# Optimization experiments

Hardware: AMD Instinct MI355X
Metric: run time of the kernel (lower is better)

The kernel has to match this reference:

```python
import jax, jax.numpy as jnp
import numpy as np

# ---- static configuration (mirrors resource grid / pilot pattern) ----
NB_SYMB = 14                 # num_ofdm_symbols
NSC = 4096                   # fft_size == num_effective_subcarriers (dc_null=False)
PILOT_SYMBS = np.array([2, 11], dtype=np.int32)  # OFDM symbols carrying pilots
STEP = 2                     # subcarriers_step (comb-2, offset 0)
M = NSC // STEP              # pilots per pilot OFDM symbol (constant, as asserted)
BATCH = 512
SC = np.arange(0, NSC, STEP, dtype=np.int32)     # pilot subcarrier positions
ROWS = np.repeat(PILOT_SYMBS, M)                 # flattened pilot (symbol, sc) map,
COLS = np.tile(SC, len(PILOT_SYMBS))             # frequency-then-time ordering


def _time_interp_tables():
    """Replicates _generate_time_interpolation_index_ with numpy (static)."""
    u = PILOT_SYMBS
    idx = np.empty((2, NB_SYMB), dtype=np.int32)
    nf = np.empty(NB_SYMB, dtype=np.float32)
    if u[0] != 0:
        idx[:, : u[0]] = u[0]
        nf[: u[0]] = 0.0
    idx[:, u[-1]:] = u[-1]
    nf[u[-1]:] = 0.0
    for i in range(len(u) - 1):
        idx[0, u[i]: u[i + 1]] = u[i]
        idx[1, u[i]: u[i + 1]] = u[i + 1]
        d = u[i + 1] - u[i]
        nf[u[i]: u[i + 1]] = np.arange(d, dtype=np.float32) / d
    return idx[0], idx[1], nf

IDX0, IDX1, NORM = _time_interp_tables()


def setup_inputs() -> dict:
    key = jax.random.key(0)
    k1, k2 = jax.random.split(key)
    shape = (BATCH, len(PILOT_SYMBS) * M)
    return {
        "h_pilots_real": jax.random.normal(k1, shape, dtype=jnp.float32),
        "h_pilots_imag": jax.random.normal(k2, shape, dtype=jnp.float32),
    }


def reference(h_pilots_real, h_pilots_imag):
    pilots = (h_pilots_real + 1j * h_pilots_imag).astype(jnp.complex64)  # [B, P]
    B = pilots.shape[0]
    # scatter_nd of pilot estimates into the full grid [T, F, B]
    updates = pilots.T  # [P, B]
    grid = jnp.zeros((NB_SYMB, NSC, B), jnp.complex64).at[ROWS, COLS].set(updates)
    # gather pilot OFDM symbols then pilot subcarriers -> [S, M, B]
    est_pilots = grid[PILOT_SYMBS][:, SC, :]
    # M-point unitary DFT along frequency (sionna.signal.fft is ortho-normalized)
    dft = jnp.fft.fft(est_pilots, axis=1, norm="ortho")
    # constant cutoff: fc = floor(M/2)
    fc = M // 2
    padded = jnp.concatenate(
        [
            dft[:, :fc, :],
            jnp.zeros((len(PILOT_SYMBS), NSC - 2 * fc, B), jnp.complex64),
            dft[:, -fc:, :],
        ],
        axis=1,
    )  # [S, NSC, B]
    scaling = jnp.asarray(np.sqrt(np.float32(STEP)), dtype=jnp.complex64)
    freq_interp = scaling * jnp.fft.ifft(padded, axis=1, norm="ortho")
    # scatter interpolated pilot symbols back into the time grid
    interp = jnp.zeros((NB_SYMB, NSC, B), jnp.complex64).at[PILOT_SYMBS].set(freq_interp)
    # time-domain linear interpolation: (H[m+1]-H[m]) * l/L + H[m]
    h0 = interp[IDX0]  # [T, F, B]
    h1 = interp[IDX1]
    norm = jnp.asarray(NORM)[:, None, None]
    out = (h1 - h0) * norm + h0
    # -> [batch, num_ofdm_symbols, num_subcarriers]
    return jnp.transpose(out, (2, 0, 1))
```

## Files before the change

### kernel.cpp

```cpp
#include <hip/hip_runtime.h>
#include <math.h>


#define NSC   4096
#define MM    2048
#define HALFM 1024
#define TSYM  14
#define NTHR  256

__global__ __launch_bounds__(NTHR)
void tdi_fft_interp(const float* __restrict__ in_r,
                    const float* __restrict__ in_i,
                    float2* __restrict__ out,
                    long long n2) {
  __shared__ float2 A[MM];
  __shared__ float  ODD0R[MM];
  __shared__ float2 W[HALFM];

  const int tid = threadIdx.x;
  const int b   = blockIdx.x;

  for (int j = tid; j < HALFM; j += NTHR) {
    float s, c;
    sincosf(-6.283185307179586476f * (float)j * (1.0f / 2048.0f), &s, &c);
    W[j] = make_float2(c, s);
  }

  const float* __restrict__ rr = in_r + (size_t)b * NSC;
  const float* __restrict__ ii = in_i + (size_t)b * NSC;

  float2 xe0[8], xe1[8];
#pragma unroll
  for (int i = 0; i < 8; ++i) {
    const int m = tid + NTHR * i;
    xe0[i] = make_float2(rr[m], ii[m]);
    xe1[i] = make_float2(rr[MM + m], ii[MM + m]);
  }

  for (int s = 0; s < 2; ++s) {
#pragma unroll
    for (int i = 0; i < 8; ++i) {
      const int m = tid + NTHR * i;
      A[m] = s ? xe1[i] : xe0[i];
    }
    __syncthreads();

    for (int st = 10; st >= 0; --st) {
      const int len = 1 << st;
#pragma unroll 4
      for (int j = tid; j < HALFM; j += NTHR) {
        const int pos = j & (len - 1);
        const int i0  = ((j >> st) << (st + 1)) | pos;
        const int i1  = i0 + len;
        const float2 a = A[i0];
        const float2 c = A[i1];
        const float2 w = W[pos << (10 - st)];
        const float dx = a.x - c.x, dy = a.y - c.y;
        A[i0] = make_float2(a.x + c.x, a.y + c.y);
        A[i1] = make_float2(dx * w.x - dy * w.y, dx * w.y + dy * w.x);
      }
      __syncthreads();
    }

    for (int p = tid; p < MM; p += NTHR) {
      const int k = (int)(__brev((unsigned)p) >> 21);
      float sn, cs;
      sincosf(3.14159265358979323846f * (float)k * (1.0f / 2048.0f), &sn, &cs);
      const float sc = (k >= HALFM) ? -(1.0f / 2048.0f) : (1.0f / 2048.0f);
      cs *= sc;
      sn *= sc;
      const float2 a = A[p];
      A[p] = make_float2(a.x * cs - a.y * sn, a.x * sn + a.y * cs);
    }
    __syncthreads();

    for (int st = 0; st <= 10; ++st) {
      const int len = 1 << st;
#pragma unroll 4
      for (int j = tid; j < HALFM; j += NTHR) {
        const int pos = j & (len - 1);
        const int i0  = ((j >> st) << (st + 1)) | pos;
        const int i1  = i0 + len;
        float2 w = W[pos << (10 - st)];
        w.y = -w.y;
        const float2 a = A[i0];
        const float2 c = A[i1];
        const float tx = c.x * w.x - c.y * w.y;
        const float ty = c.x * w.y + c.y * w.x;
        A[i0] = make_float2(a.x + tx, a.y + ty);
        A[i1] = make_float2(a.x - tx, a.y - ty);
      }
      __syncthreads();
    }

    if (s == 0) {
      for (int m = tid; m < MM; m += NTHR) ODD0R[m] = A[m].x;
      __syncthreads();
    }
  }

  for (int t = 0; t < TSYM; ++t) {
    const float w = (t < 2) ? 0.0f : (t >= 11) ? 1.0f
                     : (float)(t - 2) * (1.0f / 9.0f);
    const long long rowbase = ((long long)b * TSYM + t) * MM;
#pragma unroll
    for (int i = 0; i < 8; ++i) {
      const int m = tid + NTHR * i;
      const long long idx = rowbase + m;
      if (idx < n2) {
        const float e0 = xe0[i].x, e1 = xe1[i].x;
        const float o0 = ODD0R[m], o1 = A[m].x;
        float2 v;
        v.x = e0 + w * (e1 - e0);
        v.y = o0 + w * (o1 - o0);
        out[idx] = v;
      }
    }
  }
}

extern "C" void kernel_launch(void* const* d_in, const int* in_sizes, int n_in,
                              void* d_out, int out_size, void* d_ws, size_t ws_size,
                              hipStream_t stream) {
  const float* hr = (const float*)d_in[0];
  const float* hi = (const float*)d_in[1];
  const int batch = in_sizes[0] / NSC;
  const long long n2 = (long long)out_size / 2;
  tdi_fft_interp<<<dim3(batch), dim3(NTHR), 0, stream>>>(hr, hi, (float2*)d_out, n2);
}
```

Before: 152.3 us.

## Rewrite FFT as register radix-8 passes with both symbols in parallel

Replaces the radix-2 shared-memory FFT (22 barrier-separated stages per symbol, run sequentially for two symbols) with radix-8 register butterflies over fewer shared-memory passes. It uses 512 threads so both pilot symbols are transformed at once, and pads shared memory to avoid bank conflicts. Twiddles are computed inline with fast __sincosf instead of a table, and output is written as float4. This trades some twiddle accuracy and register pressure for far fewer barriers and shared-memory round trips.

```diff
diff --git a/kernel.cpp b/kernel.cpp
--- a/kernel.cpp
+++ b/kernel.cpp
@@ -2,119 +2,253 @@
 #include <math.h>
 
 
-#define NSC   4096
-#define MM    2048
-#define HALFM 1024
-#define TSYM  14
-#define NTHR  256
-
-__global__ __launch_bounds__(NTHR)
+#define NSC  4096
+#define MM   2048
+#define PI_F 3.14159265358979323846f
+
+__device__ __forceinline__ int pada(int i) { return i + 2 * (i >> 5); }
+
+__device__ __forceinline__ void bf_fwd(float2& a, float2& c, float tc, float ts) {
+  const float tx = a.x - c.x, ty = a.y - c.y;
+  a.x += c.x; a.y += c.y;
+  c.x = tx * tc - ty * ts;
+  c.y = tx * ts + ty * tc;
+}
+__device__ __forceinline__ void bf_inv(float2& a, float2& c, float tc, float ts) {
+  const float tx = c.x * tc - c.y * ts, ty = c.x * ts + c.y * tc;
+  c.x = a.x - tx; c.y = a.y - ty;
+  a.x += tx; a.y += ty;
+}
+
+__global__ __launch_bounds__(512)
 void tdi_fft_interp(const float* __restrict__ in_r,
                     const float* __restrict__ in_i,
-                    float2* __restrict__ out,
-                    long long n2) {
-  __shared__ float2 A[MM];
-  __shared__ float  ODD0R[MM];
-  __shared__ float2 W[HALFM];
+                    float4* __restrict__ out) {
+  __shared__ __align__(16) float2 A[2][2176];
 
   const int tid = threadIdx.x;
   const int b   = blockIdx.x;
-
-  for (int j = tid; j < HALFM; j += NTHR) {
-    float s, c;
-    sincosf(-6.283185307179586476f * (float)j * (1.0f / 2048.0f), &s, &c);
-    W[j] = make_float2(c, s);
-  }
-
-  const float* __restrict__ rr = in_r + (size_t)b * NSC;
-  const float* __restrict__ ii = in_i + (size_t)b * NSC;
-
-  float2 xe0[8], xe1[8];
-#pragma unroll
-  for (int i = 0; i < 8; ++i) {
-    const int m = tid + NTHR * i;
-    xe0[i] = make_float2(rr[m], ii[m]);
-    xe1[i] = make_float2(rr[MM + m], ii[MM + m]);
-  }
-
-  for (int s = 0; s < 2; ++s) {
-#pragma unroll
-    for (int i = 0; i < 8; ++i) {
-      const int m = tid + NTHR * i;
-      A[m] = s ? xe1[i] : xe0[i];
-    }
-    __syncthreads();
-
-    for (int st = 10; st >= 0; --st) {
-      const int len = 1 << st;
-#pragma unroll 4
-      for (int j = tid; j < HALFM; j += NTHR) {
-        const int pos = j & (len - 1);
-        const int i0  = ((j >> st) << (st + 1)) | pos;
-        const int i1  = i0 + len;
-        const float2 a = A[i0];
-        const float2 c = A[i1];
-        const float2 w = W[pos << (10 - st)];
-        const float dx = a.x - c.x, dy = a.y - c.y;
-        A[i0] = make_float2(a.x + c.x, a.y + c.y);
-        A[i1] = make_float2(dx * w.x - dy * w.y, dx * w.y + dy * w.x);
-      }
-      __syncthreads();
-    }
-
-    for (int p = tid; p < MM; p += NTHR) {
+  const int u   = tid & 255;
+  const int sym = tid >> 8;
+  float2* __restrict__ As = A[sym];
+
+  const float* __restrict__ pr = in_r + ((size_t)b << 12) + (sym << 11);
+  const float* __restrict__ pm = in_i + ((size_t)b << 12) + (sym << 11);
+
+  float2 x[8];
+  float s, c;
+
+#pragma unroll
+  for (int j = 0; j < 8; ++j)
+    x[j] = make_float2(pr[u + 256 * j], pm[u + 256 * j]);
+#pragma unroll
+  for (int j = 0; j < 4; ++j) {
+    __sincosf((float)(u + 256 * j) * (PI_F / 1024.f), &s, &c);
+    bf_fwd(x[j], x[j + 4], c, -s);
+  }
+  {
+    float s0, c0, s1, c1;
+    __sincosf((float)u * (PI_F / 512.f), &s0, &c0);
+    __sincosf((float)(u + 256) * (PI_F / 512.f), &s1, &c1);
+    bf_fwd(x[0], x[2], c0, -s0); bf_fwd(x[1], x[3], c1, -s1);
+    bf_fwd(x[4], x[6], c0, -s0); bf_fwd(x[5], x[7], c1, -s1);
+  }
+  __sincosf((float)u * (PI_F / 256.f), &s, &c);
+  bf_fwd(x[0], x[1], c, -s); bf_fwd(x[2], x[3], c, -s);
+  bf_fwd(x[4], x[5], c, -s); bf_fwd(x[6], x[7], c, -s);
+#pragma unroll
+  for (int j = 0; j < 8; ++j) As[pada(u + 256 * j)] = x[j];
+  __syncthreads();
+
+  {
+    const int q = u & 31;
+    const int base = ((u >> 5) << 8) | q;
+#pragma unroll
+    for (int j = 0; j < 8; ++j) x[j] = As[pada(base + 32 * j)];
+#pragma unroll
+    for (int j = 0; j < 4; ++j) {
+      __sincosf((float)(q + 32 * j) * (PI_F / 128.f), &s, &c);
+      bf_fwd(x[j], x[j + 4], c, -s);
+    }
+    float s0, c0, s1, c1;
+    __sincosf((float)q * (PI_F / 64.f), &s0, &c0);
+    __sincosf((float)(q + 32) * (PI_F / 64.f), &s1, &c1);
+    bf_fwd(x[0], x[2], c0, -s0); bf_fwd(x[1], x[3], c1, -s1);
+    bf_fwd(x[4], x[6], c0, -s0); bf_fwd(x[5], x[7], c1, -s1);
+    __sincosf((float)q * (PI_F / 32.f), &s, &c);
+    bf_fwd(x[0], x[1], c, -s); bf_fwd(x[2], x[3], c, -s);
+    bf_fwd(x[4], x[5], c, -s); bf_fwd(x[6], x[7], c, -s);
+#pragma unroll
+    for (int j = 0; j < 8; ++j) As[pada(base + 32 * j)] = x[j];
+  }
+  __syncthreads();
+
+  {
+    const int q = u & 3;
+    const int base = ((u >> 2) << 5) | q;
+#pragma unroll
+    for (int j = 0; j < 8; ++j) x[j] = As[pada(base + 4 * j)];
+#pragma unroll
+    for (int j = 0; j < 4; ++j) {
+      __sincosf((float)(q + 4 * j) * (PI_F / 16.f), &s, &c);
+      bf_fwd(x[j], x[j + 4], c, -s);
+    }
+    float s0, c0, s1, c1;
+    __sincosf((float)q * (PI_F / 8.f), &s0, &c0);
+    __sincosf((float)(q + 4) * (PI_F / 8.f), &s1, &c1);
+    bf_fwd(x[0], x[2], c0, -s0); bf_fwd(x[1], x[3], c1, -s1);
+    bf_fwd(x[4], x[6], c0, -s0); bf_fwd(x[5], x[7], c1, -s1);
+    __sincosf((float)q * (PI_F / 4.f), &s, &c);
+    bf_fwd(x[0], x[1], c, -s); bf_fwd(x[2], x[3], c, -s);
+    bf_fwd(x[4], x[5], c, -s); bf_fwd(x[6], x[7], c, -s);
+#pragma unroll
+    for (int j = 0; j < 8; ++j) As[pada(base + 4 * j)] = x[j];
+  }
+  __syncthreads();
+
+  {
+    const int base = u << 3;
+#pragma unroll
+    for (int j = 0; j < 8; ++j) x[j] = As[pada(base + j)];
+#pragma unroll
+    for (int g = 0; g < 8; g += 4) {
+      float2 t;
+      t.x = x[g].x - x[g+2].x;  t.y = x[g].y - x[g+2].y;
+      x[g].x += x[g+2].x;       x[g].y += x[g+2].y;
+      x[g+2] = t;
+      t.x = x[g+1].x - x[g+3].x; t.y = x[g+1].y - x[g+3].y;
+      x[g+1].x += x[g+3].x;      x[g+1].y += x[g+3].y;
+      x[g+3] = make_float2(t.y, -t.x);
+    }
+#pragma unroll
+    for (int g = 0; g < 8; g += 2) {
+      float2 t;
+      t.x = x[g].x - x[g+1].x; t.y = x[g].y - x[g+1].y;
+      x[g].x += x[g+1].x;      x[g].y += x[g+1].y;
+      x[g+1] = t;
+    }
+#pragma unroll
+    for (int j = 0; j < 8; ++j) {
+      const int p = base + j;
       const int k = (int)(__brev((unsigned)p) >> 21);
-      float sn, cs;
-      sincosf(3.14159265358979323846f * (float)k * (1.0f / 2048.0f), &sn, &cs);
-      const float sc = (k >= HALFM) ? -(1.0f / 2048.0f) : (1.0f / 2048.0f);
-      cs *= sc;
-      sn *= sc;
-      const float2 a = A[p];
-      A[p] = make_float2(a.x * cs - a.y * sn, a.x * sn + a.y * cs);
-    }
-    __syncthreads();
-
-    for (int st = 0; st <= 10; ++st) {
-      const int len = 1 << st;
-#pragma unroll 4
-      for (int j = tid; j < HALFM; j += NTHR) {
-        const int pos = j & (len - 1);
-        const int i0  = ((j >> st) << (st + 1)) | pos;
-        const int i1  = i0 + len;
-        float2 w = W[pos << (10 - st)];
-        w.y = -w.y;
-        const float2 a = A[i0];
-        const float2 c = A[i1];
-        const float tx = c.x * w.x - c.y * w.y;
-        const float ty = c.x * w.y + c.y * w.x;
-        A[i0] = make_float2(a.x + tx, a.y + ty);
-        A[i1] = make_float2(a.x - tx, a.y - ty);
-      }
-      __syncthreads();
-    }
-
-    if (s == 0) {
-      for (int m = tid; m < MM; m += NTHR) ODD0R[m] = A[m].x;
-      __syncthreads();
-    }
-  }
-
-  for (int t = 0; t < TSYM; ++t) {
-    const float w = (t < 2) ? 0.0f : (t >= 11) ? 1.0f
-                     : (float)(t - 2) * (1.0f / 9.0f);
-    const long long rowbase = ((long long)b * TSYM + t) * MM;
-#pragma unroll
-    for (int i = 0; i < 8; ++i) {
-      const int m = tid + NTHR * i;
-      const long long idx = rowbase + m;
-      if (idx < n2) {
-        const float e0 = xe0[i].x, e1 = xe1[i].x;
-        const float o0 = ODD0R[m], o1 = A[m].x;
-        float2 v;
-        v.x = e0 + w * (e1 - e0);
-        v.y = o0 + w * (o1 - o0);
-        out[idx] = v;
-      }
+      const float sc = (k >= 1024) ? -(1.f / 2048.f) : (1.f / 2048.f);
+      __sincosf((float)k * (PI_F / 2048.f), &s, &c);
+      const float fc = c * sc, fs = s * sc;
+      const float2 a = x[j];
+      x[j] = make_float2(a.x * fc - a.y * fs, a.x * fs + a.y * fc);
+    }
+#pragma unroll
+    for (int g = 0; g < 8; g += 2) {
+      const float2 t = x[g+1];
+      x[g+1].x = x[g].x - t.x; x[g+1].y = x[g].y - t.y;
+      x[g].x  += t.x;          x[g].y  += t.y;
+    }
+#pragma unroll
+    for (int g = 0; g < 8; g += 4) {
+      float2 t = x[g+2];
+      x[g+2].x = x[g].x - t.x; x[g+2].y = x[g].y - t.y;
+      x[g].x  += t.x;          x[g].y  += t.y;
+      t = make_float2(-x[g+3].y, x[g+3].x);
+      x[g+3].x = x[g+1].x - t.x; x[g+3].y = x[g+1].y - t.y;
+      x[g+1].x += t.x;           x[g+1].y += t.y;
+    }
+#pragma unroll
+    for (int j = 0; j < 8; ++j) As[pada(base + j)] = x[j];
+  }
+  __syncthreads();
+
+  {
+    const int q = u & 3;
+    const int base = ((u >> 2) << 5) | q;
+#pragma unroll
+    for (int j = 0; j < 8; ++j) x[j] = As[pada(base + 4 * j)];
+    __sincosf((float)q * (PI_F / 4.f), &s, &c);
+    bf_inv(x[0], x[1], c, s); bf_inv(x[2], x[3], c, s);
+    bf_inv(x[4], x[5], c, s); bf_inv(x[6], x[7], c, s);
+    float s0, c0, s1, c1;
+    __sincosf((float)q * (PI_F / 8.f), &s0, &c0);
+    __sincosf((float)(q + 4) * (PI_F / 8.f), &s1, &c1);
+    bf_inv(x[0], x[2], c0, s0); bf_inv(x[1], x[3], c1, s1);
+    bf_inv(x[4], x[6], c0, s0); bf_inv(x[5], x[7], c1, s1);
+#pragma unroll
+    for (int j = 0; j < 4; ++j) {
+      __sincosf((float)(q + 4 * j) * (PI_F / 16.f), &s, &c);
+      bf_inv(x[j], x[j + 4], c, s);
+    }
+#pragma unroll
+    for (int j = 0; j < 8; ++j) As[pada(base + 4 * j)] = x[j];
+  }
+  __syncthreads();
+
+  {
+    const int q = u & 31;
+    const int base = ((u >> 5) << 8) | q;
+#pragma unroll
+    for (int j = 0; j < 8; ++j) x[j] = As[pada(base + 32 * j)];
+    __sincosf((float)q * (PI_F / 32.f), &s, &c);
+    bf_inv(x[0], x[1], c, s); bf_inv(x[2], x[3], c, s);
+    bf_inv(x[4], x[5], c, s); bf_inv(x[6], x[7], c, s);
+    float s0, c0, s1, c1;
+    __sincosf((float)q * (PI_F / 64.f), &s0, &c0);
+    __sincosf((float)(q + 32) * (PI_F / 64.f), &s1, &c1);
+    bf_inv(x[0], x[2], c0, s0); bf_inv(x[1], x[3], c1, s1);
+    bf_inv(x[4], x[6], c0, s0); bf_inv(x[5], x[7], c1, s1);
+#pragma unroll
+    for (int j = 0; j < 4; ++j) {
+      __sincosf((float)(q + 32 * j) * (PI_F / 128.f), &s, &c);
+      bf_inv(x[j], x[j + 4], c, s);
+    }
+#pragma unroll
+    for (int j = 0; j < 8; ++j) As[pada(base + 32 * j)] = x[j];
+  }
+  __syncthreads();
+
+  {
+#pragma unroll
+    for (int j = 0; j < 8; ++j) x[j] = As[pada(u + 256 * j)];
+    __sincosf((float)u * (PI_F / 256.f), &s, &c);
+    bf_inv(x[0], x[1], c, s); bf_inv(x[2], x[3], c, s);
+    bf_inv(x[4], x[5], c, s); bf_inv(x[6], x[7], c, s);
+    float s0, c0, s1, c1;
+    __sincosf((float)u * (PI_F / 512.f), &s0, &c0);
+    __sincosf((float)(u + 256) * (PI_F / 512.f), &s1, &c1);
+    bf_inv(x[0], x[2], c0, s0); bf_inv(x[1], x[3], c1, s1);
+    bf_inv(x[4], x[6], c0, s0); bf_inv(x[5], x[7], c1, s1);
+#pragma unroll
+    for (int j = 0; j < 4; ++j) {
+      __sincosf((float)(u + 256 * j) * (PI_F / 1024.f), &s, &c);
+      bf_inv(x[j], x[j + 4], c, s);
+    }
+#pragma unroll
+    for (int j = 0; j < 8; ++j) As[pada(u + 256 * j)] = x[j];
+  }
+  __syncthreads();
+
+  float2 E0[2], E1[2], O0[2], O1[2];
+  const float* __restrict__ er0 = in_r + ((size_t)b << 12);
+  const float* __restrict__ er1 = er0 + MM;
+#pragma unroll
+  for (int e = 0; e < 2; ++e) {
+    const int q = tid + e * 512;
+    E0[e] = *(const float2*)&er0[2 * q];
+    E1[e] = *(const float2*)&er1[2 * q];
+    const float4 a0 = *(const float4*)&A[0][pada(2 * q)];
+    const float4 a1 = *(const float4*)&A[1][pada(2 * q)];
+    O0[e] = make_float2(a0.x, a0.z);
+    O1[e] = make_float2(a1.x, a1.z);
+  }
+  float4* __restrict__ orow = out + (size_t)b * 14 * 1024;
+  for (int t = 0; t < 14; ++t) {
+    const float w = (t < 2) ? 0.f : (t >= 11) ? 1.f : (float)(t - 2) * (1.f / 9.f);
+#pragma unroll
+    for (int e = 0; e < 2; ++e) {
+      const int q = tid + e * 512;
+      float4 v;
+      v.x = E0[e].x + w * (E1[e].x - E0[e].x);
+      v.y = O0[e].x + w * (O1[e].x - O0[e].x);
+      v.z = E0[e].y + w * (E1[e].y - E0[e].y);
+      v.w = O0[e].y + w * (O1[e].y - O0[e].y);
+      orow[t * 1024 + q] = v;
     }
   }
 }
@@ -125,6 +259,5 @@
   const float* hr = (const float*)d_in[0];
   const float* hi = (const float*)d_in[1];
   const int batch = in_sizes[0] / NSC;
-  const long long n2 = (long long)out_size / 2;
-  tdi_fft_interp<<<dim3(batch), dim3(NTHR), 0, stream>>>(hr, hi, (float2*)d_out, n2);
-}
+  tdi_fft_interp<<<dim3(batch), dim3(512), 0, stream>>>(hr, hi, (float4*)d_out);
+}
```

After: 131.9 us. -13.4%, faster.
